# Performance work log

Measured on AMD Instinct MI355X. Metric: run time of the kernel, lower is better.

## Reference

```python
import jax, jax.numpy as jnp
import numpy as np

SIZES = (1, 2, 4, 8)
C_IN = 64
KC = C_IN // 8      # key_channels = out_channels // 8 = 8
VC = C_IN           # value_channels = out_channels = 64
N_STAGES = len(SIZES)


def setup_inputs() -> dict:
    key = jax.random.key(0)
    ks = jax.random.split(key, 16)
    N, C, H, W = 1, C_IN, 64, 64
    inp = {
        "x1": jax.random.normal(ks[0], (N, C, H, W), jnp.float32),
        "x2": jax.random.normal(ks[1], (N, C, H, W), jnp.float32),
        # per-stage 1x1 conv weights (stacked over the 4 PAM stages)
        "Wq": jax.random.normal(ks[2], (N_STAGES, KC, C), jnp.float32) * 0.02,
        "bq": jnp.zeros((N_STAGES, KC), jnp.float32),
        "gammaq": 1.0 + jax.random.normal(ks[3], (N_STAGES, KC), jnp.float32) * 0.02,
        "betaq": jnp.zeros((N_STAGES, KC), jnp.float32),
        "Wk": jax.random.normal(ks[4], (N_STAGES, KC, C), jnp.float32) * 0.02,
        "bk": jnp.zeros((N_STAGES, KC), jnp.float32),
        "gammak": 1.0 + jax.random.normal(ks[5], (N_STAGES, KC), jnp.float32) * 0.02,
        "betak": jnp.zeros((N_STAGES, KC), jnp.float32),
        "Wv": jax.random.normal(ks[6], (N_STAGES, VC, C), jnp.float32) * 0.02,
        "bv": jnp.zeros((N_STAGES, VC), jnp.float32),
        # final 1x1 conv: in = C * n_stages, out = C, no bias
        "Wo": jax.random.normal(ks[7], (C, VC * N_STAGES), jnp.float32) * 0.02,
    }
    return inp


def _pam_block(x, Wq, bq, gq, betq, Wk, bk, gk, betk, Wv, bv, scale):
    # x: [N, C, H, 2W] (two images concatenated along width)
    N, C, H, W2 = x.shape
    w = W2 // 2
    kc = Wq.shape[0]

    def proj(W, b):  # 1x1 conv
        return jnp.einsum('nchw,kc->nkhw', x, W) + b[:, None, None]

    # BatchNorm (inference form: zero running mean / unit variance) folded to affine
    q = gq[:, None, None] * proj(Wq, bq) + betq[:, None, None]
    k = gk[:, None, None] * proj(Wk, bk) + betk[:, None, None]
    v = proj(Wv, bv)

    hl, wl = H // scale, w // scale

    def to_blocks(t):
        ch = t.shape[1]
        # stack left/right halves on a trailing axis: [N, ch, H, w, 2]
        t = jnp.stack([t[..., :w], t[..., w:]], axis=-1)
        # split into scale x scale spatial blocks -> [N, s*s, ch, hl*wl*2]
        t = t.reshape(N, ch, scale, hl, scale, wl, 2)
        t = t.transpose(0, 2, 4, 1, 3, 5, 6)
        return t.reshape(N, scale * scale, ch, hl * wl * 2)

    qb, kb, vb = to_blocks(q), to_blocks(k), to_blocks(v)

    sim = jnp.einsum('nbkp,nbkq->nbpq', qb, kb) * (kc ** -0.5)
    att = jax.nn.softmax(sim, axis=-1)
    # context = V @ att^T : ctx[c,p] = sum_q v[c,q] * att[p,q]
    ctx = jnp.einsum('nbcq,nbpq->nbcp', vb, att)

    Cv = Wv.shape[0]
    ctx = ctx.reshape(N, scale, scale, Cv, hl, wl, 2)
    ctx = ctx.transpose(0, 3, 1, 4, 2, 5, 6).reshape(N, Cv, H, w, 2)
    # re-concatenate the two halves along width -> [N, Cv, H, 2w]
    return jnp.concatenate([ctx[..., 0], ctx[..., 1]], axis=3)


def reference(x1, x2, Wq, bq, gammaq, betaq, Wk, bk, gammak, betak, Wv, bv, Wo):
    h_w = x1.shape[3]
    x = jnp.concatenate([x1, x2], axis=3)  # [N, C, H, 2W]
    priors = [
        _pam_block(x, Wq[i], bq[i], gammaq[i], betaq[i],
                   Wk[i], bk[i], gammak[i], betak[i],
                   Wv[i], bv[i], SIZES[i])
        for i in range(N_STAGES)
    ]
    cat = jnp.concatenate(priors, axis=1)  # [N, 4C, H, 2W]
    out = jnp.einsum('ndhw,od->nohw', cat, Wo)  # final 1x1 conv, no bias
    return out[:, :, :, :h_w], out[:, :, :, h_w:]


if __name__ == '__main__':
    o1, o2 = reference(**setup_inputs())
    print(o1.shape, o2.shape)
```

## Files before the change

### kernel.cpp

```cpp
#include <hip/hip_runtime.h>


typedef _Float16 f16x8 __attribute__((ext_vector_type(8)));
typedef float f32x16 __attribute__((ext_vector_type(16)));
typedef short bf16x8 __attribute__((ext_vector_type(8)));

__device__ __forceinline__ unsigned short f2bf(float f){
    union{float f;unsigned int i;}v; v.f=f;
    unsigned int r = v.i + 0x7fffu + ((v.i>>16)&1u);
    return (unsigned short)(r>>16);
}
__device__ __forceinline__ unsigned short f2h(float f){
    union{_Float16 h; unsigned short u;}v; v.h = (_Float16)f; return v.u;
}
__device__ __forceinline__ unsigned pack2h(float a, float b){
    auto pk = __builtin_amdgcn_cvt_pkrtz(a, b);
    unsigned u; __builtin_memcpy(&u, &pk, 4); return u;
}
__device__ __forceinline__ float exp2fast(float x){ return __builtin_amdgcn_exp2f(x); }
__device__ __forceinline__ int rfl(int x){ return __builtin_amdgcn_readfirstlane(x); }

#define QMUL 0.5100697233f

__global__ __launch_bounds__(256) void proj_all_kernel(
    const float* __restrict__ x1, const float* __restrict__ x2,
    const float* __restrict__ Wq, const float* __restrict__ bq,
    const float* __restrict__ gq, const float* __restrict__ beq,
    const float* __restrict__ Wk, const float* __restrict__ bk,
    const float* __restrict__ gk, const float* __restrict__ bek,
    const float* __restrict__ Wv, const float* __restrict__ bv,
    unsigned short* __restrict__ Qb, unsigned short* __restrict__ Kb,
    unsigned short* __restrict__ Vf)
{
    __shared__ __align__(16) float xs[64][68];
    __shared__ __align__(16) unsigned vqk[64][8];
    __shared__ __align__(16) unsigned short vv[64][64];

    const int wg = blockIdx.x, st = wg >> 8, rr = wg & 255;
    const int chunk = rr >> 1, cgrp = rr & 1;
    const int lgP = 13 - 2*st, Pm1 = (1<<lgP) - 1;
    const int hb = 6 - st, wlm = (1<<hb) - 1;
    const int t = threadIdx.x;
    const int gp0 = chunk*64;
    const int blk = gp0 >> lgP, p0 = gp0 & Pm1;
    const int si = blk >> st, sj = blk & ((1<<st)-1);
    const int hwbase = ((si<<hb)<<6) | (sj<<hb);

    for (int idx = t; idx < 4096; idx += 256) {
        int c = idx >> 6, g = idx & 63;
        int p = p0 + g, half = p & 1, pw = p >> 1;
        int hw = hwbase | ((pw>>hb)<<6) | (pw & wlm);
        xs[g][c] = (half ? x2 : x1)[c*4096 + hw];
    }
    __syncthreads();

    const int px = t & 63, wv = t >> 6;
    float xr[64];
    #pragma unroll
    for (int q4 = 0; q4 < 16; ++q4)
        *(float4*)&xr[q4*4] = *(const float4*)&xs[px][q4*4];

#define VRANGE(LO,HI)                                              \
    for (int ch = (LO); ch < (HI); ++ch) {                         \
        const int cu = rfl(st*64 + ch);                            \
        const float* wp = Wv + cu*64;                              \
        float d = bv[cu];                                          \
        _Pragma("unroll")                                          \
        for (int k = 0; k < 64; ++k) d += wp[k]*xr[k];             \
        vv[ch][px] = f2h(d);                                       \
    }
#define KPROJ(CH,DST)                                              \
    {   const int cu = rfl(st*8 + (CH));                           \
        const float* wp = Wk + cu*64;                              \
        float d = 0.f;                                             \
        _Pragma("unroll")                                          \
        for (int k = 0; k < 64; ++k) d += wp[k]*xr[k];             \
        float gm = gk[cu];                                         \
        (DST) = gm*(d + bk[cu]) + bek[cu]; }

    if (cgrp == 0) {
        if (wv == 0) {
            float qv8[8];
            for (int ch = 0; ch < 8; ++ch) {
                const int cu = rfl(st*8 + ch);
                const float* wp = Wq + cu*64;
                float d = 0.f;
                #pragma unroll
                for (int k = 0; k < 64; ++k) d += wp[k]*xr[k];
                float gm = gq[cu];
                qv8[ch] = (gm*(d + bq[cu]) + beq[cu])*QMUL;
            }
            #pragma unroll
            for (int i = 0; i < 4; ++i) vqk[px][i] = pack2h(qv8[2*i], qv8[2*i+1]);
            float k0v, k1v; KPROJ(0, k0v) KPROJ(1, k1v)
            vqk[px][4] = pack2h(k0v, k1v);
        } else if (wv == 1) {
            float ka, kb2;
            KPROJ(2, ka) KPROJ(3, kb2) vqk[px][5] = pack2h(ka, kb2);
            KPROJ(4, ka) KPROJ(5, kb2) vqk[px][6] = pack2h(ka, kb2);
            KPROJ(6, ka) KPROJ(7, kb2) vqk[px][7] = pack2h(ka, kb2);
            VRANGE(0, 4)
        } else if (wv == 2) { VRANGE(4, 14) }
        else               { VRANGE(14, 24) }
    } else {
        if      (wv == 0) { VRANGE(24, 34) }
        else if (wv == 1) { VRANGE(34, 44) }
        else if (wv == 2) { VRANGE(44, 54) }
        else              { VRANGE(54, 64) }
    }
#undef VRANGE
#undef KPROJ
    __syncthreads();

    unsigned short* Vst = Vf + st*524288 + (blk << (lgP+6));
    if (cgrp == 0) {
        if (t < 64) {
            *(uint4*)(Qb + st*65536 + (gp0 + t)*8) = *(const uint4*)&vqk[t][0];
        } else if (t < 128) {
            int p2 = t - 64;
            *(uint4*)(Kb + st*65536 + (gp0 + p2)*8) = *(const uint4*)&vqk[p2][4];
        }
        if (t < 192) {
            int ch = t >> 3, q = t & 7;
            int kb = q >> 1, lhi = q & 1;
            unsigned short tmp[8];
            #pragma unroll
            for (int u = 0; u < 8; ++u) {
                int s = q*8 + u;
                tmp[u] = vv[ch][((s&1)<<5) | (s>>1)];
            }
            *(uint4*)(Vst + p0*64 + kb*1024 + (lhi*32 + ch)*8) = *(const uint4*)tmp;
        }
    } else {
        for (int task = t; task < 320; task += 256) {
            int ch = 24 + (task >> 3), q = task & 7;
            int kb = q >> 1, lhi = q & 1;
            int b = (ch >= 32) ? 1 : 0, l31 = ch & 31;
            unsigned short tmp[8];
            #pragma unroll
            for (int u = 0; u < 8; ++u) {
                int s = q*8 + u;
                tmp[u] = vv[ch][((s&1)<<5) | (s>>1)];
            }
            *(uint4*)(Vst + p0*64 + kb*1024 + b*512 + (lhi*32 + l31)*8) = *(const uint4*)tmp;
        }
    }
}

__global__ __launch_bounds__(512) void attn_kernel(
    const unsigned short* __restrict__ Qb, const unsigned short* __restrict__ Kb,
    const unsigned short* __restrict__ Vf,
    float* __restrict__ PART, float* __restrict__ LPART)
{
    __shared__ __align__(16) float BB[8192];
    __shared__ float Lm[128];
    __shared__ float SCm[8][64];

    const int wg = blockIdx.x;
    const int t = threadIdx.x, lane = t & 63, wv = t >> 6;
    const int l31 = lane & 31, lhi = lane >> 5;

    int st, qt, slot, kbase, nkw;
    if (wg < 1024)      { st=0; qt=wg>>2; slot=wg&3;
                          kbase=(wg&3)*2048 + wv*256; nkw=256; }
    else if (wg < 1536) { int r=wg-1024; st=1; qt=r>>1; slot=4+(r&1);
                          kbase=(r&1)*1024 + wv*128;  nkw=128; }
    else if (wg < 1792) { st=2; qt=wg-1536; slot=6; kbase=wv*64; nkw=64; }
    else                { st=3; qt=wg-1792; slot=7; kbase=wv*64;
                          nkw=(wv<2)?64:0; }

    const int lgP = 13 - 2*st, P = 1 << lgP;
    const int blk = qt >> (lgP - 5);
    const int q0  = (qt & ((P>>5)-1)) * 32;

    const unsigned short* Qg = Qb + st*65536 + blk*P*8;
    const unsigned short* Kg = Kb + st*65536 + blk*P*8;
    const unsigned short* Vg = Vf + st*524288 + blk*P*64;

    f16x8 qb = *(const f16x8*)(Qg + (q0 + l31)*8);

    f32x16 acc0, acc1;
    #pragma unroll
    for (int r = 0; r < 16; ++r) { acc0[r] = 0.f; acc1[r] = 0.f; }
    float rs[4];
    #pragma unroll
    for (int r = 0; r < 4; ++r) rs[r] = 0.f;

    for (int k0 = kbase; k0 < kbase + nkw; k0 += 64) {
        f16x8 ka0, ka1;
        #pragma unroll
        for (int j = 0; j < 8; ++j) { ka0[j] = (_Float16)0.f; ka1[j] = (_Float16)0.f; }
        if (lane < 32) {
            ka0 = *(const f16x8*)(Kg + (k0 + l31)*8);
            ka1 = *(const f16x8*)(Kg + (k0 + 32 + l31)*8);
        }
        f32x16 S0, S1;
        #pragma unroll
        for (int r = 0; r < 16; ++r) { S0[r] = 0.f; S1[r] = 0.f; }
        S0 = __builtin_amdgcn_mfma_f32_32x32x16_f16(ka0, qb, S0, 0, 0, 0);
        S1 = __builtin_amdgcn_mfma_f32_32x32x16_f16(ka1, qb, S1, 0, 0, 0);

        unsigned pw[16];
        #pragma unroll
        for (int r = 0; r < 16; ++r) {
            float e0 = exp2fast(S0[r]);
            float e1 = exp2fast(S1[r]);
            rs[r & 3] += e0 + e1;
            pw[r] = pack2h(e0, e1);
        }

        #pragma unroll
        for (int kc = 0; kc < 4; ++kc) {
            f16x8 pb;
            __builtin_memcpy(&pb, &pw[kc*4], 16);
            const unsigned short* vbase = Vg + (k0 + kc*16)*64;
            f16x8 vb0 = *(const f16x8*)(vbase + lane*8);
            f16x8 vb1 = *(const f16x8*)(vbase + 512 + lane*8);
            acc0 = __builtin_amdgcn_mfma_f32_32x32x16_f16(pb, vb0, acc0, 0, 0, 0);
            acc1 = __builtin_amdgcn_mfma_f32_32x32x16_f16(pb, vb1, acc1, 0, 0, 0);
        }
    }

    float lsum = rs[0] + rs[1] + rs[2] + rs[3];
    SCm[wv][lhi*32 + l31] = lsum;
    __syncthreads();
    float lsum_reg = 0.f;
    if (lane < 32) lsum_reg = SCm[wv][l31] + SCm[wv][32 + l31];

    if (wv < 4) {
        float* B = BB + wv*2048;
        #pragma unroll
        for (int r = 0; r < 16; ++r) {
            int qrow = (r&3) + 8*(r>>2) + 4*lhi;
            B[qrow*64 + l31]      = acc0[r];
            B[qrow*64 + 32 + l31] = acc1[r];
        }
        if (lane < 32) Lm[wv*32 + l31] = lsum_reg;
    }
    __syncthreads();
    if (wv >= 4) {
        float* B = BB + (wv-4)*2048;
        #pragma unroll
        for (int r = 0; r < 16; ++r) {
            int qrow = (r&3) + 8*(r>>2) + 4*lhi;
            B[qrow*64 + l31]      += acc0[r];
            B[qrow*64 + 32 + l31] += acc1[r];
        }
        if (lane < 32) Lm[(wv-4)*32 + l31] += lsum_reg;
    }
    __syncthreads();

    float4* Pslab4 = (float4*)(PART + slot*524288 + qt*2048);
    const float4* B4 = (const float4*)BB;
    {
        float4 a = B4[t], b = B4[t+512], c = B4[t+1024], d = B4[t+1536];
        Pslab4[t] = float4{a.x+b.x+c.x+d.x, a.y+b.y+c.y+d.y,
                           a.z+b.z+c.z+d.z, a.w+b.w+c.w+d.w};
    }
    if (t < 32)
        LPART[slot*8192 + qt*32 + t] = Lm[t] + Lm[32+t] + Lm[64+t] + Lm[96+t];
}

__global__ __launch_bounds__(256) void normconv_kernel(
    const float* __restrict__ PART, const float* __restrict__ LPART,
    const float* __restrict__ Wo, float* __restrict__ out)
{
    __shared__ __align__(16) unsigned short csb[32][264];
    __shared__ __align__(16) unsigned short wof[16384];
    __shared__ float voutf[64][33];
    __shared__ float linv[4][32];
    __shared__ int gpar[4][32];
    const int t = threadIdx.x;
    const int px0 = blockIdx.x * 32;

    {
        int oc = t >> 2, d0 = (t & 3) * 64;
        for (int b = 0; b < 8; ++b) {
            int d = d0 + b*8;
            float4 w0 = *(const float4*)(Wo + oc*256 + d);
            float4 w1 = *(const float4*)(Wo + oc*256 + d + 4);
            unsigned short tmp[8];
            tmp[0]=f2bf(w0.x); tmp[1]=f2bf(w0.y); tmp[2]=f2bf(w0.z); tmp[3]=f2bf(w0.w);
            tmp[4]=f2bf(w1.x); tmp[5]=f2bf(w1.y); tmp[6]=f2bf(w1.z); tmp[7]=f2bf(w1.w);
            *(uint4*)&wof[(d>>3)*512 + oc*8] = *(const uint4*)tmp;
        }
    }
    if (t < 128) {
        const int s0tab[4] = {0,4,6,7};
        const int sctab[4] = {4,2,1,1};
        int stt = t >> 5, i = t & 31;
        int pix = px0 + i;
        int half = pix >> 12, hw = pix & 4095;
        int h = hw >> 6, w = hw & 63;
        int hb = 6 - stt, wlm = (1<<hb)-1;
        int si = h >> hb, sj = w >> hb, hi = h & wlm, wi = w & wlm;
        int blk = (si << stt) | sj;
        int p = (((hi << hb) | wi) << 1) | half;
        int gp = blk*(8192>>(2*stt)) + p;
        gpar[stt][i] = gp;
        int s0 = s0tab[stt];
        float l = LPART[s0*8192 + gp];
        for (int c = 1; c < sctab[stt]; ++c) l += LPART[(s0+c)*8192 + gp];
        linv[stt][i] = 1.f / l;
    }
    __syncthreads();

    {
        const int s0tab[4] = {0,4,6,7};
        const int sctab[4] = {4,2,1,1};
        int gpx = t >> 3, cvg = (t & 7) * 8;
        for (int stt = 0; stt < 4; ++stt) {
            int gp = gpar[stt][gpx];
            const float* p = PART + s0tab[stt]*524288
                           + (gp>>5)*2048 + (gp&31)*64 + cvg;
            float4 a = *(const float4*)p;
            float4 b = *(const float4*)(p + 4);
            for (int c = 1; c < sctab[stt]; ++c) {
                float4 a2 = *(const float4*)(p + c*524288);
                float4 b2 = *(const float4*)(p + c*524288 + 4);
                a.x+=a2.x; a.y+=a2.y; a.z+=a2.z; a.w+=a2.w;
                b.x+=b2.x; b.y+=b2.y; b.z+=b2.z; b.w+=b2.w;
            }
            float li = linv[stt][gpx];
            unsigned short tmp[8];
            tmp[0]=f2bf(a.x*li); tmp[1]=f2bf(a.y*li); tmp[2]=f2bf(a.z*li); tmp[3]=f2bf(a.w*li);
            tmp[4]=f2bf(b.x*li); tmp[5]=f2bf(b.y*li); tmp[6]=f2bf(b.z*li); tmp[7]=f2bf(b.w*li);
            *(uint4*)&csb[gpx][stt*64 + cvg] = *(const uint4*)tmp;
        }
    }
    __syncthreads();

    const int lane = t & 63, wvv = t >> 6;
    const int l31 = lane & 31, lhi = lane >> 5;
    const int nh = wvv & 1, kh = wvv >> 1;
    f32x16 acc;
    #pragma unroll
    for (int r = 0; r < 16; ++r) acc[r] = 0.f;
    #pragma unroll
    for (int s = 0; s < 8; ++s) {
        int dg = kh*16 + s*2 + lhi;
        bf16x8 a = *(const bf16x8*)&csb[l31][kh*128 + s*16 + 8*lhi];
        bf16x8 b = *(const bf16x8*)&wof[dg*512 + (nh*32 + l31)*8];
        acc = __builtin_amdgcn_mfma_f32_32x32x16_bf16(a, b, acc, 0, 0, 0);
    }
    if (kh == 0) {
        #pragma unroll
        for (int r = 0; r < 16; ++r)
            voutf[nh*32 + l31][(r&3) + 8*(r>>2) + 4*lhi] = acc[r];
    }
    __syncthreads();
    if (kh == 1) {
        #pragma unroll
        for (int r = 0; r < 16; ++r)
            voutf[nh*32 + l31][(r&3) + 8*(r>>2) + 4*lhi] += acc[r];
    }
    __syncthreads();

    const int half = px0 >> 12, hw0 = px0 & 4095;
    float* obase = out + half*262144 + hw0;
    #pragma unroll
    for (int r = 0; r < 8; ++r) {
        int idx = t + r*256;
        int oc = idx >> 5, pxi = idx & 31;
        obase[oc*4096 + pxi] = voutf[oc][pxi];
    }
}

extern "C" void kernel_launch(void* const* d_in, const int* in_sizes, int n_in,
                              void* d_out, int out_size, void* d_ws, size_t ws_size,
                              hipStream_t stream)
{
    (void)out_size; (void)ws_size;
    const float *x1, *x2, *Wq, *bq, *gq, *beq, *Wk, *bk, *gk, *bek, *Wv, *bv, *Wo;

    if (n_in >= 13 && in_sizes[0] == 2048) {
        Wk  = (const float*)d_in[0];  Wo  = (const float*)d_in[1];
        Wq  = (const float*)d_in[2];  Wv  = (const float*)d_in[3];
        bek = (const float*)d_in[4];  beq = (const float*)d_in[5];
        bk  = (const float*)d_in[6];  bq  = (const float*)d_in[7];
        bv  = (const float*)d_in[8];  gk  = (const float*)d_in[9];
        gq  = (const float*)d_in[10];
        x1  = (const float*)d_in[11]; x2  = (const float*)d_in[12];
    } else {
        x1  = (const float*)d_in[0];  x2  = (const float*)d_in[1];
        Wq  = (const float*)d_in[2];  bq  = (const float*)d_in[3];
        gq  = (const float*)d_in[4];  beq = (const float*)d_in[5];
        Wk  = (const float*)d_in[6];  bk  = (const float*)d_in[7];
        gk  = (const float*)d_in[8];  bek = (const float*)d_in[9];
        Wv  = (const float*)d_in[10]; bv  = (const float*)d_in[11];
        Wo  = (const float*)d_in[12];
    }

    unsigned short* Qb = (unsigned short*)d_ws;
    unsigned short* Kb = Qb + 262144;
    unsigned short* Vf = Kb + 262144;
    float* PART  = (float*)d_ws + 1310720;
    float* LPART = PART + 4194304;

    proj_all_kernel<<<1024, 256, 0, stream>>>(x1,x2,Wq,bq,gq,beq,Wk,bk,gk,bek,Wv,bv,Qb,Kb,Vf);
    attn_kernel<<<2048, 512, 0, stream>>>(Qb,Kb,Vf,PART,LPART);
    normconv_kernel<<<256, 256, 0, stream>>>(PART, LPART, Wo, (float*)d_out);
}
```

Before: 132.5 us.

## Repartition attention into 256-thread blocks with more split-K slots and templated loops

```diff
diff --git a/kernel.cpp b/kernel.cpp
--- a/kernel.cpp
+++ b/kernel.cpp
@@ -147,53 +147,24 @@
     }
 }
 
-__global__ __launch_bounds__(512) void attn_kernel(
-    const unsigned short* __restrict__ Qb, const unsigned short* __restrict__ Kb,
-    const unsigned short* __restrict__ Vf,
-    float* __restrict__ PART, float* __restrict__ LPART)
+template<int NITER>
+__device__ __forceinline__ void attn_core(
+    const unsigned short* __restrict__ Kg,
+    const unsigned short* __restrict__ Vg,
+    int kbase, f16x8 qb, int lane, unsigned msk,
+    f32x16& acc0, f32x16& acc1, float* rs)
 {
-    __shared__ __align__(16) float BB[8192];
-    __shared__ float Lm[128];
-    __shared__ float SCm[8][64];
-
-    const int wg = blockIdx.x;
-    const int t = threadIdx.x, lane = t & 63, wv = t >> 6;
-    const int l31 = lane & 31, lhi = lane >> 5;
-
-    int st, qt, slot, kbase, nkw;
-    if (wg < 1024)      { st=0; qt=wg>>2; slot=wg&3;
-                          kbase=(wg&3)*2048 + wv*256; nkw=256; }
-    else if (wg < 1536) { int r=wg-1024; st=1; qt=r>>1; slot=4+(r&1);
-                          kbase=(r&1)*1024 + wv*128;  nkw=128; }
-    else if (wg < 1792) { st=2; qt=wg-1536; slot=6; kbase=wv*64; nkw=64; }
-    else                { st=3; qt=wg-1792; slot=7; kbase=wv*64;
-                          nkw=(wv<2)?64:0; }
-
-    const int lgP = 13 - 2*st, P = 1 << lgP;
-    const int blk = qt >> (lgP - 5);
-    const int q0  = (qt & ((P>>5)-1)) * 32;
-
-    const unsigned short* Qg = Qb + st*65536 + blk*P*8;
-    const unsigned short* Kg = Kb + st*65536 + blk*P*8;
-    const unsigned short* Vg = Vf + st*524288 + blk*P*64;
-
-    f16x8 qb = *(const f16x8*)(Qg + (q0 + l31)*8);
-
-    f32x16 acc0, acc1;
-    #pragma unroll
-    for (int r = 0; r < 16; ++r) { acc0[r] = 0.f; acc1[r] = 0.f; }
-    float rs[4];
-    #pragma unroll
-    for (int r = 0; r < 4; ++r) rs[r] = 0.f;
-
-    for (int k0 = kbase; k0 < kbase + nkw; k0 += 64) {
+    const int l31 = lane & 31;
+    for (int it = 0; it < NITER; ++it) {
+        const int k0 = kbase + it*64;
+        uint4 ku0 = *(const uint4*)(Kg + (k0 + l31)*8);
+        uint4 ku1 = *(const uint4*)(Kg + (k0 + 32 + l31)*8);
+        ku0.x &= msk; ku0.y &= msk; ku0.z &= msk; ku0.w &= msk;
+        ku1.x &= msk; ku1.y &= msk; ku1.z &= msk; ku1.w &= msk;
         f16x8 ka0, ka1;
-        #pragma unroll
-        for (int j = 0; j < 8; ++j) { ka0[j] = (_Float16)0.f; ka1[j] = (_Float16)0.f; }
-        if (lane < 32) {
-            ka0 = *(const f16x8*)(Kg + (k0 + l31)*8);
-            ka1 = *(const f16x8*)(Kg + (k0 + 32 + l31)*8);
-        }
+        __builtin_memcpy(&ka0, &ku0, 16);
+        __builtin_memcpy(&ka1, &ku1, 16);
+
         f32x16 S0, S1;
         #pragma unroll
         for (int r = 0; r < 16; ++r) { S0[r] = 0.f; S1[r] = 0.f; }
@@ -220,14 +191,51 @@
             acc1 = __builtin_amdgcn_mfma_f32_32x32x16_f16(pb, vb1, acc1, 0, 0, 0);
         }
     }
-
-    float lsum = rs[0] + rs[1] + rs[2] + rs[3];
-    SCm[wv][lhi*32 + l31] = lsum;
-    __syncthreads();
-    float lsum_reg = 0.f;
-    if (lane < 32) lsum_reg = SCm[wv][l31] + SCm[wv][32 + l31];
-
-    if (wv < 4) {
+}
+
+__global__ __launch_bounds__(256, 4) void attn_kernel(
+    const unsigned short* __restrict__ Qb, const unsigned short* __restrict__ Kb,
+    const unsigned short* __restrict__ Vf,
+    float* __restrict__ PART, float* __restrict__ LPART)
+{
+    __shared__ __align__(16) float BB[8192];
+    __shared__ float SCm[4][64];
+
+    const int wg = blockIdx.x;
+    const int t = threadIdx.x, lane = t & 63, wv = t >> 6;
+    const int l31 = lane & 31, lhi = lane >> 5;
+
+    int st, qt, slot, kbase, mode;
+    if (wg < 2048)      { st=0; qt=wg>>3; slot=wg&7;
+                          kbase=(wg&7)*1024 + wv*256; mode=4; }
+    else if (wg < 2560) { int r=wg-2048; st=1; qt=r>>1; slot=8+(r&1);
+                          kbase=(r&1)*1024 + wv*256;  mode=4; }
+    else if (wg < 2816) { st=2; qt=wg-2560; slot=10; kbase=wv*128; mode=2; }
+    else                { st=3; qt=wg-2816; slot=11; kbase=wv*64;
+                          mode=(wv<2)?1:0; }
+
+    const int lgP = 13 - 2*st, P = 1 << lgP;
+    const int blk = qt >> (lgP - 5);
+    const int q0  = (qt & ((P>>5)-1)) * 32;
+
+    const unsigned short* Qg = Qb + st*65536 + blk*P*8;
+    const unsigned short* Kg = Kb + st*65536 + blk*P*8;
+    const unsigned short* Vg = Vf + st*524288 + blk*P*64;
+
+    f16x8 qb = *(const f16x8*)(Qg + (q0 + l31)*8);
+    const unsigned msk = (lane < 32) ? 0xFFFFFFFFu : 0u;
+
+    f32x16 acc0, acc1;
+    #pragma unroll
+    for (int r = 0; r < 16; ++r) { acc0[r] = 0.f; acc1[r] = 0.f; }
+    float rs[4] = {0.f, 0.f, 0.f, 0.f};
+
+    if      (mode == 4) attn_core<4>(Kg, Vg, kbase, qb, lane, msk, acc0, acc1, rs);
+    else if (mode == 2) attn_core<2>(Kg, Vg, kbase, qb, lane, msk, acc0, acc1, rs);
+    else if (mode == 1) attn_core<1>(Kg, Vg, kbase, qb, lane, msk, acc0, acc1, rs);
+
+    SCm[wv][lane] = rs[0] + rs[1] + rs[2] + rs[3];
+    {
         float* B = BB + wv*2048;
         #pragma unroll
         for (int r = 0; r < 16; ++r) {
@@ -235,30 +243,22 @@
             B[qrow*64 + l31]      = acc0[r];
             B[qrow*64 + 32 + l31] = acc1[r];
         }
-        if (lane < 32) Lm[wv*32 + l31] = lsum_reg;
-    }
-    __syncthreads();
-    if (wv >= 4) {
-        float* B = BB + (wv-4)*2048;
-        #pragma unroll
-        for (int r = 0; r < 16; ++r) {
-            int qrow = (r&3) + 8*(r>>2) + 4*lhi;
-            B[qrow*64 + l31]      += acc0[r];
-            B[qrow*64 + 32 + l31] += acc1[r];
-        }
-        if (lane < 32) Lm[(wv-4)*32 + l31] += lsum_reg;
     }
     __syncthreads();
 
     float4* Pslab4 = (float4*)(PART + slot*524288 + qt*2048);
     const float4* B4 = (const float4*)BB;
-    {
-        float4 a = B4[t], b = B4[t+512], c = B4[t+1024], d = B4[t+1536];
-        Pslab4[t] = float4{a.x+b.x+c.x+d.x, a.y+b.y+c.y+d.y,
-                           a.z+b.z+c.z+d.z, a.w+b.w+c.w+d.w};
+    #pragma unroll
+    for (int r = 0; r < 2; ++r) {
+        int idx = t + r*256;
+        float4 a = B4[idx], b = B4[idx+512], c = B4[idx+1024], d = B4[idx+1536];
+        Pslab4[idx] = float4{a.x+b.x+c.x+d.x, a.y+b.y+c.y+d.y,
+                             a.z+b.z+c.z+d.z, a.w+b.w+c.w+d.w};
     }
     if (t < 32)
-        LPART[slot*8192 + qt*32 + t] = Lm[t] + Lm[32+t] + Lm[64+t] + Lm[96+t];
+        LPART[slot*8192 + qt*32 + t] =
+            (SCm[0][t] + SCm[0][32+t]) + (SCm[1][t] + SCm[1][32+t])
+          + (SCm[2][t] + SCm[2][32+t]) + (SCm[3][t] + SCm[3][32+t]);
 }
 
 __global__ __launch_bounds__(256) void normconv_kernel(
@@ -286,8 +286,8 @@
         }
     }
     if (t < 128) {
-        const int s0tab[4] = {0,4,6,7};
-        const int sctab[4] = {4,2,1,1};
+        const int s0tab[4] = {0,8,10,11};
+        const int sctab[4] = {8,2,1,1};
         int stt = t >> 5, i = t & 31;
         int pix = px0 + i;
         int half = pix >> 12, hw = pix & 4095;
@@ -306,8 +306,8 @@
     __syncthreads();
 
     {
-        const int s0tab[4] = {0,4,6,7};
-        const int sctab[4] = {4,2,1,1};
+        const int s0tab[4] = {0,8,10,11};
+        const int sctab[4] = {8,2,1,1};
         int gpx = t >> 3, cvg = (t & 7) * 8;
         for (int stt = 0; stt < 4; ++stt) {
             int gp = gpar[stt][gpx];
@@ -395,9 +395,9 @@
     unsigned short* Kb = Qb + 262144;
     unsigned short* Vf = Kb + 262144;
     float* PART  = (float*)d_ws + 1310720;
-    float* LPART = PART + 4194304;
+    float* LPART = PART + 6291456;
 
     proj_all_kernel<<<1024, 256, 0, stream>>>(x1,x2,Wq,bq,gq,beq,Wk,bk,gk,bek,Wv,bv,Qb,Kb,Vf);
-    attn_kernel<<<2048, 512, 0, stream>>>(Qb,Kb,Vf,PART,LPART);
+    attn_kernel<<<3072, 256, 0, stream>>>(Qb,Kb,Vf,PART,LPART);
     normconv_kernel<<<256, 256, 0, stream>>>(PART, LPART, Wo, (float*)d_out);
 }
```

Result: no change. 133.5 us (+0.8%).
